# Optimization experiments

Measured on AMD Instinct MI355X. Metric: run time of the kernel, lower is better.

## Reference

```python
import jax, jax.numpy as jnp
import numpy as np

# static config (matches init_kwargs)
C = 64            # dim_split = dim // 4
DIM = 256
HID = 128         # int(dim//4 * mlp_ratio), mlp_ratio=2
S = 64            # state_dim
NH, HD = 16, 4    # GA: num_heads = C // head_dim, head_dim = 4
AK, AP = 11, 5    # att_kernel, att_padding
B, H, W = 8, 28, 28


def conv2d(x, w, pad, stride=1, groups=1, bias=None):
    out = jax.lax.conv_general_dilated(
        x, w, (stride, stride), pad, feature_group_count=groups,
        dimension_numbers=('NCHW', 'OIHW', 'NCHW'))
    if bias is not None:
        out = out + bias[None, :, None, None]
    return out


def pw(x, w, b=None):  # 1x1 conv, w: (O, Cin)
    y = jnp.einsum('oc,bchw->bohw', w, x)
    return y if b is None else y + b[None, :, None, None]


def bn(x, p, eps=1e-5):  # eval-mode BatchNorm2d; p: (4, C) = gamma, beta, mean, var
    g, b, m, v = p
    s = g / jnp.sqrt(v + eps)
    return (x - m[None, :, None, None]) * s[None, :, None, None] + b[None, :, None, None]


def relu6(x):
    return jnp.minimum(jax.nn.relu(x), 6.0)


def maxpool3(x):  # 3x3, stride 1, pad 1
    return jax.lax.reduce_window(x, -jnp.inf, jax.lax.max, (1, 1, 3, 3), (1, 1, 1, 1),
                                 [(0, 0), (0, 0), (1, 1), (1, 1)])


def blurpool(x):  # antialiased_cnns.BlurPool(channels, stride=3), filt_size=4
    a = np.array([1.0, 3.0, 3.0, 1.0])
    filt = np.outer(a, a)
    filt = filt / filt.sum()
    c = x.shape[1]
    w = jnp.asarray(np.tile(filt[None, None], (c, 1, 1, 1)), x.dtype)
    xp = jnp.pad(x, ((0, 0), (0, 0), (1, 2), (1, 2)), mode='reflect')
    return conv2d(xp, w, [(0, 0), (0, 0)], stride=3, groups=c)


def h_transform(x):
    b, c, hs, ws = x.shape
    x = jnp.pad(x, ((0, 0), (0, 0), (0, 0), (0, ws))).reshape(b, c, -1)[..., :-ws]
    return x.reshape(b, c, hs, 2 * ws - 1)


def inv_h_transform(x):
    b, c, hs, _ = x.shape
    x = jnp.pad(x.reshape(b, c, -1), ((0, 0), (0, 0), (0, hs)))
    return x.reshape(b, c, hs, 2 * hs)[..., :hs]


def v_transform(x):
    return h_transform(x.transpose(0, 1, 3, 2)).transpose(0, 1, 3, 2)


def inv_v_transform(x):
    return inv_h_transform(x.transpose(0, 1, 3, 2)).transpose(0, 1, 3, 2)


def _forward(x, dw1_w, dw1_b, bn_dw1, f1_w, f1_b, f2_w, f2_b, g_w, g_b, bn_g,
             dw2_w, dw2_b, hatt1_w, vatt1_w, hatt2_w, vatt2_w, bn_mra,
             bcdt_w, ssd_dw_w, hz_w, out_w, A_param, D_param,
             qkv_w, proj_w, bn_norm4, mlp1_w, bn_mlp, mlp2_w, bn_norm1):
    shortcut = x
    x1, x2, x3, x4 = jnp.split(x, 4, axis=1)

    # --- branch 1: dwconv + star-gated MLP ---
    x1o = bn(conv2d(x1, dw1_w, [(3, 3), (3, 3)], groups=C, bias=dw1_b), bn_dw1)
    x1 = relu6(pw(x1o, f1_w, f1_b)) * pw(x1o, f2_w, f2_b)
    x1 = conv2d(bn(pw(x1, g_w, g_b), bn_g), dw2_w, [(3, 3), (3, 3)], groups=C, bias=dw2_b)

    # --- branch 2: MRA ---
    xt = blurpool(maxpool3(x2))  # (B, C, 10, 10)
    xh1 = conv2d(xt, hatt1_w, [(AP, AP), (1, 1)], groups=C)
    xw1 = conv2d(xt, vatt1_w, [(1, 1), (AP, AP)], groups=C)
    xh2 = inv_h_transform(conv2d(h_transform(xt), hatt2_w, [(AP, AP), (1, 1)], groups=C))
    xw2 = inv_v_transform(conv2d(v_transform(xt), vatt2_w, [(1, 1), (AP, AP)], groups=C))
    att = jax.nn.sigmoid(bn(xh1 + xw1 + xh2 + xw2, bn_mra))
    hs, ws = att.shape[-2], att.shape[-1]
    ri = (jnp.arange(H) * hs) // H  # nearest-neighbor upsampling indices
    ci = (jnp.arange(W) * ws) // W
    x2 = x2 * att[:, :, ri][:, :, :, ci]

    # --- branch 3: HSMSSD (hidden-state-mixer SSD) ---
    L = H * W
    xs = x3.reshape(B, C, L)
    bcdt = conv2d(jnp.einsum('oc,bcl->bol', bcdt_w, xs).reshape(B, 3 * S, H, W),
                  ssd_dw_w, [(1, 1), (1, 1)], groups=3 * S).reshape(B, 3 * S, L)
    Bm, Cm, dt = jnp.split(bcdt, 3, axis=1)              # each (B, S, L)
    A = jax.nn.softmax(dt + A_param[None, :, None], axis=-1)
    h = jnp.einsum('bcl,bsl->bcs', xs, A * Bm)           # (B, C, S)
    h_, z = jnp.split(jnp.einsum('oc,bcs->bos', hz_w, h), 2, axis=1)
    h_ = jnp.einsum('oc,bcs->bos', out_w, h_ * jax.nn.silu(z) + h_ * D_param)
    x3 = jnp.einsum('bcs,bsl->bcl', h_, Cm).reshape(B, C, H, W)

    # --- branch 4: GA full attention + BN residual (stage == 3) ---
    t = x4.reshape(B, C, L).transpose(0, 2, 1)           # (B, N, C)
    qkv = (t @ qkv_w.T).reshape(B, L, 3, NH, HD).transpose(2, 0, 3, 1, 4)
    q, k, v = qkv[0], qkv[1], qkv[2]
    attn = jax.nn.softmax(jnp.einsum('bhnd,bhmd->bhnm', q, k) * HD ** -0.5, axis=-1)
    o = jnp.einsum('bhnm,bhmd->bhnd', attn, v).transpose(0, 2, 1, 3).reshape(B, L, NH * HD)
    x4 = bn(x4 + (o @ proj_w.T).transpose(0, 2, 1).reshape(B, C, H, W), bn_norm4)

    # --- merge + MLP ---
    xa = jnp.concatenate([x1, x2, x3, x4], axis=1)
    m = pw(jax.nn.relu(bn(pw(xa, mlp1_w), bn_mlp)), mlp2_w)
    return shortcut + bn(m, bn_norm1)


def setup_inputs() -> dict:
    key = jax.random.key(0)
    ks = iter(jax.random.split(key, 64))

    def w(shape, s=0.05):
        return jax.random.normal(next(ks), shape, dtype=jnp.float32) * s

    def bnp(c):
        g = 1.0 + 0.1 * jax.random.normal(next(ks), (c,), dtype=jnp.float32)
        b = 0.1 * jax.random.normal(next(ks), (c,), dtype=jnp.float32)
        m = 0.1 * jax.random.normal(next(ks), (c,), dtype=jnp.float32)
        v = 0.5 + jax.random.uniform(next(ks), (c,), dtype=jnp.float32)
        return jnp.stack([g, b, m, v])

    return dict(
        x=jax.random.normal(next(ks), (B, DIM, H, W), dtype=jnp.float32),
        dw1_w=w((C, 1, 7, 7), 0.1), dw1_b=w((C,), 0.02), bn_dw1=bnp(C),
        f1_w=w((HID, C)), f1_b=w((HID,), 0.02),
        f2_w=w((HID, C)), f2_b=w((HID,), 0.02),
        g_w=w((C, HID)), g_b=w((C,), 0.02), bn_g=bnp(C),
        dw2_w=w((C, 1, 7, 7), 0.1), dw2_b=w((C,), 0.02),
        hatt1_w=w((C, 1, AK, 3), 0.1), vatt1_w=w((C, 1, 3, AK), 0.1),
        hatt2_w=w((C, 1, AK, 3), 0.1), vatt2_w=w((C, 1, 3, AK), 0.1),
        bn_mra=bnp(C),
        bcdt_w=w((3 * S, C)), ssd_dw_w=w((3 * S, 1, 3, 3), 0.1),
        hz_w=w((2 * C, C)), out_w=w((C, C)),
        A_param=jax.random.uniform(next(ks), (S,), dtype=jnp.float32, minval=1.0, maxval=16.0),
        D_param=jnp.ones((1,), dtype=jnp.float32),
        qkv_w=w((3 * NH * HD, C)), proj_w=w((C, NH * HD)),
        bn_norm4=bnp(C),
        mlp1_w=w((HID, DIM)), bn_mlp=bnp(HID), mlp2_w=w((DIM, HID)),
        bn_norm1=bnp(DIM),
    )


def reference(x, dw1_w, dw1_b, bn_dw1, f1_w, f1_b, f2_w, f2_b, g_w, g_b, bn_g,
              dw2_w, dw2_b, hatt1_w, vatt1_w, hatt2_w, vatt2_w, bn_mra,
              bcdt_w, ssd_dw_w, hz_w, out_w, A_param, D_param,
              qkv_w, proj_w, bn_norm4, mlp1_w, bn_mlp, mlp2_w, bn_norm1):
    return _forward(x, dw1_w, dw1_b, bn_dw1, f1_w, f1_b, f2_w, f2_b, g_w, g_b, bn_g,
                    dw2_w, dw2_b, hatt1_w, vatt1_w, hatt2_w, vatt2_w, bn_mra,
                    bcdt_w, ssd_dw_w, hz_w, out_w, A_param, D_param,
                    qkv_w, proj_w, bn_norm4, mlp1_w, bn_mlp, mlp2_w, bn_norm1)
```

## Files before the change

kernel.cpp:

```cpp
#include <hip/hip_runtime.h>
#include <hip/hip_bf16.h>
#include <math.h>

#define DEV __device__ __forceinline__

constexpr int B=8, C=64, DIM=256, HID=128, S=64, NH=16, HD=4, LPIX=784;
constexpr int NPIX = B*LPIX;
constexpr int CH   = (NPIX+255)/256;
constexpr int QB   = 12*((NPIX+511)/512);

constexpr size_t OFF_X1O = 0;
constexpr size_t OFF_T1  = OFF_X1O + (size_t)B*C*LPIX;
constexpr size_t OFF_T2  = OFF_T1  + (size_t)B*HID*LPIX;
constexpr size_t OFF_XA  = OFF_T2  + (size_t)B*C*LPIX;
constexpr size_t OFF_BC2 = OFF_XA  + (size_t)B*DIM*LPIX;
constexpr size_t OFF_WGT = OFF_BC2 + (size_t)B*192*LPIX;
constexpr size_t OFF_H   = OFF_WGT + (size_t)B*S*LPIX;
constexpr size_t OFF_HO  = OFF_H   + (size_t)4*B*C*S;
constexpr size_t OFF_QKV = OFF_HO  + (size_t)B*C*S;
constexpr size_t OFF_O   = OFF_QKV + (size_t)3*B*NH*LPIX*HD;
constexpr size_t OFF_LS  = OFF_O   + (size_t)4*B*LPIX*C;
constexpr size_t OFF_MID = OFF_LS  + (size_t)4*B*NH*LPIX;

DEV float bnorm(float x, const float* p, int c, int nc){
  float g=p[c], bb=p[nc+c], m=p[2*nc+c], v=p[3*nc+c];
  return (x-m)*(g*rsqrtf(v+1e-5f))+bb;
}
DEV int refl(int p){ int k=p-1; if(k<0)k=-k; if(k>27)k=54-k; return k; }

DEV bool upix(int blk, int tid, int ngroups, int& grp, int& b, int& l){
  grp = blk % ngroups;
  int gidx = (blk/ngroups)*256 + tid;
  if(gidx >= NPIX) return false;
  b = gidx / LPIX; l = gidx % LPIX;
  return true;
}

DEV void body_dw1t(int bc, int tid, float* xs, const float* X, const float* w, const float* bias, const float* bnp, float* out){
  int c = bc & 63, b = bc >> 6;
  const float* xp = X + ((size_t)(b*DIM+c))*LPIX;
  for(int i=tid;i<34*34;i+=256) xs[i]=0.f;
  __syncthreads();
  for(int i=tid;i<LPIX;i+=256){ int y=i/28, x=i%28; xs[(y+3)*34+(x+3)]=xp[i]; }
  __syncthreads();
  const float* wc = w + (size_t)c*49;
  float bs = bias[c];
  for(int i=tid;i<LPIX;i+=256){
    int y=i/28, x=i%28;
    float s = bs;
    #pragma unroll
    for(int ky=0;ky<7;ky++){
      #pragma unroll
      for(int kx=0;kx<7;kx++)
        s += xs[(y+ky)*34 + x+kx]*wc[ky*7+kx];
    }
    out[((size_t)(b*C+c))*LPIX + i] = bnorm(s,bnp,c,C);
  }
}

DEV void body_branch2(int bc, int tid, float* smem, const float* X,
                      const float* h1w,const float* v1w,const float* h2w,const float* v2w,
                      const float* bnp, float* xa){
  int c = bc & 63, b = bc >> 6;
  float* xs  = smem;
  float* mp  = smem+LPIX;
  float* xt  = smem+2*LPIX;
  float* attv= smem+2*LPIX+100;
  const float* xp = X + ((size_t)(b*DIM+64+c))*LPIX;
  for(int i=tid;i<LPIX;i+=256) xs[i]=xp[i];
  __syncthreads();
  for(int i=tid;i<LPIX;i+=256){
    int y=i/28, x=i%28;
    float m=-1e30f;
    for(int dy=-1;dy<=1;dy++){ int iy=y+dy; if(iy<0||iy>=28) continue;
      for(int dx=-1;dx<=1;dx++){ int ix=x+dx; if(ix<0||ix>=28) continue;
        m=fmaxf(m,xs[iy*28+ix]); } }
    mp[i]=m;
  }
  __syncthreads();
  if(tid<100){
    int ii=tid/10, j=tid%10;
    const float fw[4]={0.125f,0.375f,0.375f,0.125f};
    float s=0;
    for(int ky=0;ky<4;ky++){ int rr=refl(3*ii+ky);
      for(int kx=0;kx<4;kx++){ int cc=refl(3*j+kx);
        s += fw[ky]*fw[kx]*mp[rr*28+cc]; } }
    xt[tid]=s;
  }
  __syncthreads();
  if(tid<100){
    int r=tid/10, j=tid%10;
    float s=0;
    for(int kh=0;kh<11;kh++){ int a=r+kh-5; if(a<0||a>=10) continue;
      for(int kw=0;kw<3;kw++){ int b2=j+kw-1; if(b2<0||b2>=10) continue;
        s+=xt[a*10+b2]*h1w[(size_t)c*33+kh*3+kw]; } }
    for(int kh=0;kh<3;kh++){ int a=r+kh-1; if(a<0||a>=10) continue;
      for(int kw=0;kw<11;kw++){ int b2=j+kw-5; if(b2<0||b2>=10) continue;
        s+=xt[a*10+b2]*v1w[(size_t)c*33+kh*11+kw]; } }
    { int t=20*r+j; int r2=t/19, j2=t%19;
      for(int kh=0;kh<11;kh++){ int a=r2+kh-5; if(a<0||a>=10) continue;
        for(int kw=0;kw<3;kw++){ int b2=j2+kw-1; if(b2<0||b2>=19) continue;
          int i2=19*a+b2; int row=i2/20, col=i2%20;
          if(col<10) s+=xt[row*10+col]*h2w[(size_t)c*33+kh*3+kw]; } } }
    { int t=20*j+r; int p=t%19, q=t/19;
      for(int kh=0;kh<3;kh++){ int a=p+kh-1; if(a<0||a>=19) continue;
        for(int kw=0;kw<11;kw++){ int b2=q+kw-5; if(b2<0||b2>=10) continue;
          int i2=19*b2+a; int row=i2/20, col=i2%20;
          if(col<10) s+=xt[col*10+row]*v2w[(size_t)c*33+kh*11+kw]; } } }
    s = bnorm(s,bnp,c,C);
    attv[tid] = 1.f/(1.f+__expf(-s));
  }
  __syncthreads();
  float* dst = xa + ((size_t)(b*DIM+64+c))*LPIX;
  for(int i=tid;i<LPIX;i+=256){
    int y=i/28, x=i%28;
    float a = attv[((y*10)/28)*10 + (x*10)/28];
    dst[i] = xs[i]*a;
  }
}

DEV void body_qkv(int blk, int tid, const float* X, const float* w, float* qkvb){
  int og = blk % 12;
  int p0 = (blk/12)*512 + tid;
  if(p0 >= NPIX) return;
  int o0 = og*16;
  int b0 = p0/LPIX, l0 = p0%LPIX;
  int p1 = p0 + 256;
  bool has1 = p1 < NPIX;
  int b1 = has1 ? p1/LPIX : b0, l1 = has1 ? p1%LPIX : l0;
  const float* xp0 = X + ((size_t)(b0*DIM+192))*LPIX + l0;
  const float* xp1 = X + ((size_t)(b1*DIM+192))*LPIX + l1;
  float s0[16], s1[16];
  #pragma unroll
  for(int t=0;t<16;t++){ s0[t]=0.f; s1[t]=0.f; }
  for(int c=0;c<C;c+=4){
    float a0=xp0[(size_t)c*LPIX],     a1=xp0[(size_t)(c+1)*LPIX],
          a2=xp0[(size_t)(c+2)*LPIX], a3=xp0[(size_t)(c+3)*LPIX];
    float e0=xp1[(size_t)c*LPIX],     e1=xp1[(size_t)(c+1)*LPIX],
          e2=xp1[(size_t)(c+2)*LPIX], e3=xp1[(size_t)(c+3)*LPIX];
    #pragma unroll
    for(int t=0;t<16;t++){
      const float* wr = w + (size_t)(o0+t)*C + c;
      float w0=wr[0], w1=wr[1], w2=wr[2], w3=wr[3];
      s0[t] += w0*a0 + w1*a1 + w2*a2 + w3*a3;
      s1[t] += w0*e0 + w1*e1 + w2*e2 + w3*e3;
    }
  }
  int which=o0>>6, head0=(o0&63)>>2;
  #pragma unroll
  for(int t4=0;t4<4;t4++){
    float4* dst = (float4*)(qkvb + (size_t)which*B*NH*LPIX*HD + ((size_t)((b0*NH+head0+t4)*LPIX+l0))*HD);
    *dst = make_float4(s0[4*t4],s0[4*t4+1],s0[4*t4+2],s0[4*t4+3]);
  }
  if(has1){
    #pragma unroll
    for(int t4=0;t4<4;t4++){
      float4* dst = (float4*)(qkvb + (size_t)which*B*NH*LPIX*HD + ((size_t)((b1*NH+head0+t4)*LPIX+l1))*HD);
      *dst = make_float4(s1[4*t4],s1[4*t4+1],s1[4*t4+2],s1[4*t4+3]);
    }
  }
}

DEV void body_bcdtssd(int blk, int tid, float* smem, const float* X, const float* w, const float* dww,
                      float* bc2, float* wgt){
  int b = blk/48, og = blk%48; int o0=og*4;
  float* bc1s = smem;
  float* dts  = smem + 4*LPIX;
  const float* xp = X + ((size_t)(b*DIM+128))*LPIX;
  {
    int l0=tid, l1=tid+256, l2=tid+512;
    float acc0[4]={0,0,0,0}, acc1[4]={0,0,0,0}, acc2[4]={0,0,0,0};
    for(int c=0;c<C;c+=4){
      float x00=xp[(size_t)c*LPIX+l0],     x01=xp[(size_t)(c+1)*LPIX+l0],
            x02=xp[(size_t)(c+2)*LPIX+l0], x03=xp[(size_t)(c+3)*LPIX+l0];
      float x10=xp[(size_t)c*LPIX+l1],     x11=xp[(size_t)(c+1)*LPIX+l1],
            x12=xp[(size_t)(c+2)*LPIX+l1], x13=xp[(size_t)(c+3)*LPIX+l1];
      float x20=xp[(size_t)c*LPIX+l2],     x21=xp[(size_t)(c+1)*LPIX+l2],
            x22=xp[(size_t)(c+2)*LPIX+l2], x23=xp[(size_t)(c+3)*LPIX+l2];
      #pragma unroll
      for(int t=0;t<4;t++){
        const float* wr = w + (size_t)(o0+t)*C + c;
        float w0=wr[0], w1=wr[1], w2=wr[2], w3=wr[3];
        acc0[t] += w0*x00 + w1*x01 + w2*x02 + w3*x03;
        acc1[t] += w0*x10 + w1*x11 + w2*x12 + w3*x13;
        acc2[t] += w0*x20 + w1*x21 + w2*x22 + w3*x23;
      }
    }
    #pragma unroll
    for(int t=0;t<4;t++){
      bc1s[t*LPIX+l0]=acc0[t];
      bc1s[t*LPIX+l1]=acc1[t];
      bc1s[t*LPIX+l2]=acc2[t];
    }
    if(tid<16){
      int l=768+tid;
      float a0=0,a1=0,a2=0,a3=0;
      for(int c=0;c<C;c+=4){
        float x0=xp[(size_t)c*LPIX+l],     x1=xp[(size_t)(c+1)*LPIX+l],
              x2=xp[(size_t)(c+2)*LPIX+l], x3=xp[(size_t)(c+3)*LPIX+l];
        const float* w0p = w + (size_t)(o0+0)*C + c;
        const float* w1p = w + (size_t)(o0+1)*C + c;
        const float* w2p = w + (size_t)(o0+2)*C + c;
        const float* w3p = w + (size_t)(o0+3)*C + c;
        a0 += w0p[0]*x0 + w0p[1]*x1 + w0p[2]*x2 + w0p[3]*x3;
        a1 += w1p[0]*x0 + w1p[1]*x1 + w1p[2]*x2 + w1p[3]*x3;
        a2 += w2p[0]*x0 + w2p[1]*x1 + w2p[2]*x2 + w2p[3]*x3;
        a3 += w3p[0]*x0 + w3p[1]*x1 + w3p[2]*x2 + w3p[3]*x3;
      }
      bc1s[0*LPIX+l]=a0; bc1s[1*LPIX+l]=a1; bc1s[2*LPIX+l]=a2; bc1s[3*LPIX+l]=a3;
    }
  }
  __syncthreads();
  for(int i=tid;i<4*LPIX;i+=256){
    int oo=i/LPIX, l=i%LPIX; int y=l/28, x=l%28;
    const float* p = bc1s + oo*LPIX;
    const float* wk = dww + (size_t)(o0+oo)*9;
    float s=0;
    for(int ky=0;ky<3;ky++){ int iy=y+ky-1; if(iy<0||iy>=28) continue;
      for(int kx=0;kx<3;kx++){ int ix=x+kx-1; if(ix<0||ix>=28) continue;
        s += p[iy*28+ix]*wk[ky*3+kx]; } }
    dts[i] = s;
    bc2[((size_t)(b*192+o0+oo))*LPIX + l] = s;
  }
  if(og >= 32){
    __syncthreads();
    int wv = tid>>6, lane = tid&63;
    float* row = dts + wv*LPIX;
    float mx = -1e30f;
    for(int l=lane;l<LPIX;l+=64) mx = fmaxf(mx, row[l]);
    for(int off=32;off;off>>=1) mx = fmaxf(mx, __shfl_xor(mx,off));
    float sum=0;
    for(int l=lane;l<LPIX;l+=64){ float e=__expf(row[l]-mx); row[l]=e; sum+=e; }
    for(int off=32;off;off>>=1) sum += __shfl_xor(sum,off);
    float inv = 1.f/sum;
    int s_ = o0-128+wv;
    float* wp = wgt + ((size_t)(b*S+s_))*LPIX;
    for(int l=lane;l<LPIX;l+=64) wp[l] = row[l]*inv;
  }
}

DEV void body_attn(int blk, int tid, float4* ks, float4* vs, const float* qkvb,
                   float* ob, float* lsb){
  int bh = blk >> 2, ms = blk & 3;
  int b = bh>>4, h = bh&15;
  const float4* q4 = (const float4*)(qkvb + (size_t)bh*LPIX*HD);
  const float4* k4 = (const float4*)(qkvb + (size_t)(B*NH + bh)*LPIX*HD) + ms*196;
  const float4* v4 = (const float4*)(qkvb + (size_t)(2*B*NH + bh)*LPIX*HD) + ms*196;
  for(int i=tid;i<196;i+=256){ ks[i]=k4[i]; vs[i]=v4[i]; }
  __syncthreads();
  const float SC = 0.5f*1.44269504f;
  float* obp = ob + (size_t)ms*B*LPIX*C;
  float* lsq = lsb + (size_t)ms*B*NH*LPIX + (size_t)bh*LPIX;

  float4 q[3];
  #pragma unroll
  for(int j=0;j<3;j++){
    float4 t = q4[tid + 256*j];
    q[j] = make_float4(t.x*SC, t.y*SC, t.z*SC, t.w*SC);
  }
  float l0[3]={0,0,0}, l1[3]={0,0,0};
  float ax0[3]={0,0,0}, ax1[3]={0,0,0};
  float ay0[3]={0,0,0}, ay1[3]={0,0,0};
  float az0[3]={0,0,0}, az1[3]={0,0,0};
  float aw0[3]={0,0,0}, aw1[3]={0,0,0};
  for(int m=0;m<196;m+=2){
    float4 k0=ks[m], k1=ks[m+1];
    float4 v0=vs[m], v1=vs[m+1];
    #pragma unroll
    for(int j=0;j<3;j++){
      float s0 = q[j].x*k0.x + q[j].y*k0.y + q[j].z*k0.z + q[j].w*k0.w;
      float s1 = q[j].x*k1.x + q[j].y*k1.y + q[j].z*k1.z + q[j].w*k1.w;
      float p0 = __builtin_amdgcn_exp2f(s0);
      float p1 = __builtin_amdgcn_exp2f(s1);
      l0[j]+=p0;        l1[j]+=p1;
      ax0[j]+=p0*v0.x;  ax1[j]+=p1*v1.x;
      ay0[j]+=p0*v0.y;  ay1[j]+=p1*v1.y;
      az0[j]+=p0*v0.z;  az1[j]+=p1*v1.z;
      aw0[j]+=p0*v0.w;  aw1[j]+=p1*v1.w;
    }
  }
  #pragma unroll
  for(int j=0;j<3;j++){
    int r = tid + 256*j;
    *(float4*)(obp + ((size_t)(b*LPIX+r))*C + h*4) =
        make_float4(ax0[j]+ax1[j], ay0[j]+ay1[j], az0[j]+az1[j], aw0[j]+aw1[j]);
    lsq[r] = l0[j]+l1[j];
  }
  if(tid < 16){
    int r = 768 + tid;
    float4 t = q4[r];
    float4 qq = make_float4(t.x*SC,t.y*SC,t.z*SC,t.w*SC);
    float ls=0; float4 a=make_float4(0,0,0,0);
    for(int m=0;m<196;m++){
      float4 kv=ks[m], vv=vs[m];
      float sc = qq.x*kv.x+qq.y*kv.y+qq.z*kv.z+qq.w*kv.w;
      float p = __builtin_amdgcn_exp2f(sc);
      ls+=p; a.x+=p*vv.x; a.y+=p*vv.y; a.z+=p*vv.z; a.w+=p*vv.w;
    }
    *(float4*)(obp + ((size_t)(b*LPIX+r))*C + h*4) = a;
    lsq[r] = ls;
  }
}

DEV void body_star(int blk, int tid, const float* x1o, const float* f1w,const float* f1b,const float* f2w,const float* f2b,float* t1){
  int jg, b, l; if(!upix(blk, tid, 32, jg, b, l)) return;
  int j0=jg*4;
  const float* xp = x1o + (size_t)b*C*LPIX + l;
  float a[4], g[4];
  for(int t=0;t<4;t++){ a[t]=f1b[j0+t]; g[t]=f2b[j0+t]; }
  for(int c=0;c<C;c++){
    float xv = xp[(size_t)c*LPIX];
    for(int t=0;t<4;t++){ a[t]+=f1w[(size_t)(j0+t)*C+c]*xv; g[t]+=f2w[(size_t)(j0+t)*C+c]*xv; }
  }
  for(int t=0;t<4;t++){
    float av = fminf(fmaxf(a[t],0.f),6.f);
    t1[((size_t)(b*HID+j0+t))*LPIX + l] = av*g[t];
  }
}

DEV void body_gproj(int blk, int tid, const float* t1, const float* gw,const float* gb,const float* bnp,float* t2){
  int cg, b, l; if(!upix(blk, tid, 4, cg, b, l)) return;
  int c0=cg*16;
  const float* tp = t1 + (size_t)b*HID*LPIX + l;
  float s[16];
  #pragma unroll
  for(int t=0;t<16;t++) s[t]=gb[c0+t];
  for(int j=0;j<HID;j++){
    float xv = tp[(size_t)j*LPIX];
    #pragma unroll
    for(int t=0;t<16;t++) s[t]+=gw[(size_t)(c0+t)*HID+j]*xv;
  }
  #pragma unroll
  for(int t=0;t<16;t++) t2[((size_t)(b*C+c0+t))*LPIX + l]=bnorm(s[t],bnp,c0+t,C);
}

DEV void body_x4(int blk, int tid, const float* X, const float* ob, const float* lsb,
                 const float* projw, const float* bnp, float* xa){
  int cg, b, l; if(!upix(blk, tid, 4, cg, b, l)) return;
  int c0=cg*16;
  const float* p0 = ob + ((size_t)(b*LPIX+l))*C;
  const float* p1 = p0 + (size_t)B*LPIX*C;
  const float* p2 = p1 + (size_t)B*LPIX*C;
  const float* p3 = p2 + (size_t)B*LPIX*C;
  float s[16];
  #pragma unroll
  for(int t=0;t<16;t++) s[t]=0.f;
  for(int h=0;h<NH;h++){
    size_t li = ((size_t)(b*NH+h))*LPIX + l;
    float lsum = lsb[li] + lsb[(size_t)B*NH*LPIX+li] + lsb[(size_t)2*B*NH*LPIX+li] + lsb[(size_t)3*B*NH*LPIX+li];
    float iv = 1.f/lsum;
    float4 q0=*(const float4*)(p0+h*4), q1=*(const float4*)(p1+h*4),
           q2=*(const float4*)(p2+h*4), q3=*(const float4*)(p3+h*4);
    float ov0=(q0.x+q1.x+q2.x+q3.x)*iv;
    float ov1=(q0.y+q1.y+q2.y+q3.y)*iv;
    float ov2=(q0.z+q1.z+q2.z+q3.z)*iv;
    float ov3=(q0.w+q1.w+q2.w+q3.w)*iv;
    const float* pw = projw + h*4;
    #pragma unroll
    for(int t=0;t<16;t++){
      const float* pr = pw + (size_t)(c0+t)*C;
      s[t] += pr[0]*ov0 + pr[1]*ov1 + pr[2]*ov2 + pr[3]*ov3;
    }
  }
  #pragma unroll
  for(int t=0;t<16;t++){
    float v = s[t] + X[((size_t)(b*DIM+192+c0+t))*LPIX + l];
    xa[((size_t)(b*DIM+192+c0+t))*LPIX + l] = bnorm(v,bnp,c0+t,C);
  }
}

DEV void body_h(int blk, int tid, float* smem, const float* X, const float* wgt, const float* bc2, float* hq){
  int b = blk >> 6, sub = blk & 63;
  int tile = sub >> 2, qq = sub & 3;
  int ct = (tile>>2)*16, st = (tile&3)*16;
  int l0 = qq*196;
  float (*Xs)[197] = (float(*)[197])smem;
  float (*Ws)[197] = (float(*)[197])(smem + 16*197);
  for(int i=tid;i<16*196;i+=256){
    int r=i/196, col=i%196;
    Xs[r][col] = X[((size_t)(b*DIM+128+ct+r))*LPIX + l0 + col];
    Ws[r][col] = wgt[((size_t)(b*S+st+r))*LPIX + l0 + col]
               * bc2[((size_t)(b*192+st+r))*LPIX + l0 + col];
  }
  __syncthreads();
  int tc = tid>>4, ts = tid&15;
  float acc=0;
  #pragma unroll 4
  for(int l=0;l<196;l++) acc += Xs[tc][l]*Ws[ts][l];
  hq[(size_t)qq*B*C*S + ((size_t)(b*C+ct+tc))*S + st+ts] = acc;
}

DEV void body_dw2t(int bc, int tid, float* xs, const float* t2, const float* w, const float* bias, float* xa){
  int c = bc & 63, b = bc >> 6;
  const float* tp = t2 + ((size_t)(b*C+c))*LPIX;
  for(int i=tid;i<34*34;i+=256) xs[i]=0.f;
  __syncthreads();
  for(int i=tid;i<LPIX;i+=256){ int y=i/28, x=i%28; xs[(y+3)*34+(x+3)]=tp[i]; }
  __syncthreads();
  const float* wc = w + (size_t)c*49;
  float bs = bias[c];
  for(int i=tid;i<LPIX;i+=256){
    int y=i/28, x=i%28;
    float s = bs;
    #pragma unroll
    for(int ky=0;ky<7;ky++){
      #pragma unroll
      for(int kx=0;kx<7;kx++)
        s += xs[(y+ky)*34 + x+kx]*wc[ky*7+kx];
    }
    xa[((size_t)(b*DIM+c))*LPIX + i] = s;
  }
}

DEV void body_mixho(int blk, int tid, float* smem, const float* hq, const float* hzw,
                    const float* Dp, const float* outw, float* ho){
  int b = blk >> 3, st = (blk & 7) * 8;
  float (*hs2)[8] = (float(*)[8])smem;
  float (*g1s)[8] = (float(*)[8])(smem + C*8);
  for(int i=tid;i<C*8;i+=256){
    int k=i>>3, si=i&7;
    size_t off = ((size_t)(b*C+k))*S + st + si;
    hs2[k][si] = hq[off] + hq[(size_t)B*C*S+off] + hq[(size_t)2*B*C*S+off] + hq[(size_t)3*B*C*S+off];
  }
  __syncthreads();
  float D = Dp[0];
  for(int i=tid;i<C*8;i+=256){
    int c=i>>3, si=i&7;
    float hv=0, zv=0;
    for(int k=0;k<C;k++){ float x=hs2[k][si]; hv+=hzw[(size_t)c*C+k]*x; zv+=hzw[(size_t)(C+c)*C+k]*x; }
    float sil = zv/(1.f+__expf(-zv));
    g1s[c][si]=hv*sil+hv*D;
  }
  __syncthreads();
  for(int i=tid;i<C*8;i+=256){
    int c=i>>3, si=i&7;
    float acc=0;
    for(int k=0;k<C;k++) acc+=outw[(size_t)c*C+k]*g1s[k][si];
    ho[((size_t)(b*C+c))*S + st + si]=acc;
  }
}

DEV void body_x3(int blk, int tid, const float* ho, const float* bc2, float* xa){
  int cg, b, l; if(!upix(blk, tid, 16, cg, b, l)) return;
  int c0=cg*4;
  const float* hp = ho + (size_t)(b*C+c0)*S;
  const float* cm = bc2 + ((size_t)(b*192+64))*LPIX + l;
  float s[4]={0,0,0,0};
  for(int s_=0;s_<S;s_++){
    float cv = cm[(size_t)s_*LPIX];
    for(int t=0;t<4;t++) s[t] += hp[(size_t)t*S+s_]*cv;
  }
  for(int t=0;t<4;t++)
    xa[((size_t)(b*DIM+128+c0+t))*LPIX + l] = s[t];
}

__global__ void k_s1(const float* X,
                     const float* bcdt_w, const float* ssd_dw, float* bc2, float* wgt,
                     const float* h1w,const float* v1w,const float* h2w,const float* v2w,const float* bn_mra,
                     const float* qkv_w, float* qkvb,
                     const float* dw1_w,const float* dw1_b,const float* bn_dw1,
                     float* xa, float* x1o){
  __shared__ float smem[8*LPIX];
  int blk = blockIdx.x, tid = threadIdx.x;
  if(blk < 384)            body_bcdtssd(blk, tid, smem, X, bcdt_w, ssd_dw, bc2, wgt);
  else if(blk < 896)       body_branch2(blk-384, tid, smem, X, h1w,v1w,h2w,v2w, bn_mra, xa);
  else if(blk < 896+QB)    body_qkv(blk-896, tid, X, qkv_w, qkvb);
  else                     body_dw1t(blk-(896+QB), tid, smem, X, dw1_w, dw1_b, bn_dw1, x1o);
}

__global__ void k_s2(const float* qkvb, float* ob, float* lsb,
                     const float* x1o, const float* f1w,const float* f1b,const float* f2w,const float* f2b, float* t1,
                     const float* X, const float* wgt, const float* bc2, float* hq){
  __shared__ float4 smem4[1576];
  float* smem = (float*)smem4;
  int blk = blockIdx.x, tid = threadIdx.x;
  if(blk < 512)            body_attn(blk, tid, smem4, smem4+196, qkvb, ob, lsb);
  else if(blk < 512+32*CH) body_star(blk-512, tid, x1o, f1w,f1b,f2w,f2b, t1);
  else                     body_h(blk-(512+32*CH), tid, smem, X, wgt, bc2, hq);
}

__global__ void k_s3(const float* t1, const float* gw,const float* gb,const float* bn_g, float* t2,
                     const float* X, const float* ob, const float* lsb,
                     const float* projw, const float* bn_n4, float* xa,
                     const float* hq, const float* hzw, const float* Dp, const float* outw, float* ho){
  __shared__ float smem[2*C*8];
  int blk = blockIdx.x, tid = threadIdx.x;
  if(blk < 64)           body_mixho(blk, tid, smem, hq, hzw, Dp, outw, ho);
  else if(blk < 64+4*CH) body_gproj(blk-64, tid, t1, gw, gb, bn_g, t2);
  else                   body_x4(blk-(64+4*CH), tid, X, ob, lsb, projw, bn_n4, xa);
}

__global__ void k_s4(const float* t2, const float* dw2_w, const float* dw2_b, float* xa,
                     const float* ho, const float* bc2){
  __shared__ float smem[34*34];
  int blk = blockIdx.x, tid = threadIdx.x;
  if(blk < 512) body_dw2t(blk, tid, smem, t2, dw2_w, dw2_b, xa);
  else          body_x3(blk-512, tid, ho, bc2, xa);
}

__global__ void k_mid(const float* xa, const float* m1w, const float* bnp, float* mid){
  int jg, b, l; if(!upix(blockIdx.x, threadIdx.x, 32, jg, b, l)) return;
  int j0=jg*4;
  const float* xp = xa + (size_t)b*DIM*LPIX + l;
  float s[4]={0,0,0,0};
  for(int c=0;c<DIM;c++){
    float xv=xp[(size_t)c*LPIX];
    for(int t=0;t<4;t++) s[t]+=m1w[(size_t)(j0+t)*DIM+c]*xv;
  }
  for(int t=0;t<4;t++)
    mid[((size_t)(b*HID+j0+t))*LPIX + l] = fmaxf(bnorm(s[t],bnp,j0+t,HID),0.f);
}

__global__ void k_out(const float* X, const float* mid, const float* m2w, const float* bnp, float* out){
  int cg, b, l; if(!upix(blockIdx.x, threadIdx.x, 32, cg, b, l)) return;
  int c0=cg*8;
  const float* mp_ = mid + (size_t)b*HID*LPIX + l;
  float s[8]={0,0,0,0,0,0,0,0};
  for(int j=0;j<HID;j++){
    float mv=mp_[(size_t)j*LPIX];
    for(int t=0;t<8;t++) s[t]+=m2w[(size_t)(c0+t)*HID+j]*mv;
  }
  for(int t=0;t<8;t++){
    size_t oi = ((size_t)(b*DIM+c0+t))*LPIX + l;
    out[oi] = bnorm(s[t],bnp,c0+t,DIM) + X[oi];
  }
}

extern "C" void kernel_launch(void* const* d_in, const int* in_sizes, int n_in,
                              void* d_out, int out_size, void* d_ws, size_t ws_size,
                              hipStream_t stream) {
  const float* X      = (const float*)d_in[0];
  const float* dw1_w  = (const float*)d_in[1];
  const float* dw1_b  = (const float*)d_in[2];
  const float* bn_dw1 = (const float*)d_in[3];
  const float* f1_w   = (const float*)d_in[4];
  const float* f1_b   = (const float*)d_in[5];
  const float* f2_w   = (const float*)d_in[6];
  const float* f2_b   = (const float*)d_in[7];
  const float* g_w    = (const float*)d_in[8];
  const float* g_b    = (const float*)d_in[9];
  const float* bn_g   = (const float*)d_in[10];
  const float* dw2_w  = (const float*)d_in[11];
  const float* dw2_b  = (const float*)d_in[12];
  const float* hatt1w = (const float*)d_in[13];
  const float* vatt1w = (const float*)d_in[14];
  const float* hatt2w = (const float*)d_in[15];
  const float* vatt2w = (const float*)d_in[16];
  const float* bn_mra = (const float*)d_in[17];
  const float* bcdt_w = (const float*)d_in[18];
  const float* ssd_dw = (const float*)d_in[19];
  const float* hz_w   = (const float*)d_in[20];
  const float* out_w  = (const float*)d_in[21];
  const float* D_p    = (const float*)d_in[23];
  const float* qkv_w  = (const float*)d_in[24];
  const float* proj_w = (const float*)d_in[25];
  const float* bn_n4  = (const float*)d_in[26];
  const float* mlp1_w = (const float*)d_in[27];
  const float* bn_mlp = (const float*)d_in[28];
  const float* mlp2_w = (const float*)d_in[29];
  const float* bn_n1  = (const float*)d_in[30];

  float* ws   = (float*)d_ws;
  float* x1o  = ws+OFF_X1O;  float* t1  = ws+OFF_T1;  float* t2  = ws+OFF_T2;
  float* xa   = ws+OFF_XA;   float* bc2 = ws+OFF_BC2; float* wgt = ws+OFF_WGT;
  float* hq   = ws+OFF_H;    float* ho  = ws+OFF_HO;  float* qkvb= ws+OFF_QKV;
  float* ob   = ws+OFF_O;    float* lsb = ws+OFF_LS;  float* mid = ws+OFF_MID;

  dim3 blk(256);

  k_s1 <<<dim3(896+QB+512),blk,0,stream>>>(X, bcdt_w, ssd_dw, bc2, wgt,
                                     hatt1w,vatt1w,hatt2w,vatt2w,bn_mra,
                                     qkv_w, qkvb, dw1_w,dw1_b,bn_dw1, xa, x1o);
  k_s2 <<<dim3(512+32*CH+512),blk,0,stream>>>(qkvb, ob, lsb,
                                     x1o, f1_w,f1_b,f2_w,f2_b, t1,
                                     X, wgt, bc2, hq);
  k_s3 <<<dim3(64+8*CH),blk,0,stream>>>(t1, g_w,g_b,bn_g, t2,
                                     X, ob, lsb, proj_w, bn_n4, xa,
                                     hq, hz_w, D_p, out_w, ho);
  k_s4 <<<dim3(512+16*CH),blk,0,stream>>>(t2, dw2_w, dw2_b, xa, ho, bc2);
  k_mid<<<dim3(32*CH),blk,0,stream>>>(xa,mlp1_w,bn_mlp,mid);
  k_out<<<dim3(32*CH),blk,0,stream>>>(X,mid,mlp2_w,bn_n1,(float*)d_out);
}
```

Measured before the change: 283.4 us.

## Shrink shared memory and add launch bounds to raise k_s1/k_s2 occupancy

In the bcdt/ssd body, the softmax rows are now computed one at a time with block-wide max and sum reductions. This lets that stage use about 5 rows of shared memory instead of 8. The body_h GEMM tile is split into two 98-column halves so k_s2 needs half the shared buffer. Both kernels get __launch_bounds__(256,8) so more blocks fit per CU. The trade-offs are extra __syncthreads in the softmax and tile loops, and a risk of register spills under the tighter register cap.

```diff
diff --git a/kernel.cpp b/kernel.cpp
--- a/kernel.cpp
+++ b/kernel.cpp
@@ -165,7 +165,8 @@
                       float* bc2, float* wgt){
   int b = blk/48, og = blk%48; int o0=og*4;
   float* bc1s = smem;
-  float* dts  = smem + 4*LPIX;
+  float* dts1 = smem + 4*LPIX;
+  float* red  = smem + 5*LPIX;
   const float* xp = X + ((size_t)(b*DIM+128))*LPIX;
   {
     int l0=tid, l1=tid+256, l2=tid+512;
@@ -211,31 +212,50 @@
     }
   }
   __syncthreads();
-  for(int i=tid;i<4*LPIX;i+=256){
-    int oo=i/LPIX, l=i%LPIX; int y=l/28, x=l%28;
-    const float* p = bc1s + oo*LPIX;
-    const float* wk = dww + (size_t)(o0+oo)*9;
-    float s=0;
-    for(int ky=0;ky<3;ky++){ int iy=y+ky-1; if(iy<0||iy>=28) continue;
-      for(int kx=0;kx<3;kx++){ int ix=x+kx-1; if(ix<0||ix>=28) continue;
-        s += p[iy*28+ix]*wk[ky*3+kx]; } }
-    dts[i] = s;
-    bc2[((size_t)(b*192+o0+oo))*LPIX + l] = s;
-  }
-  if(og >= 32){
-    __syncthreads();
+  if(og < 32){
+    for(int i=tid;i<4*LPIX;i+=256){
+      int oo=i/LPIX, l=i%LPIX; int y=l/28, x=l%28;
+      const float* p = bc1s + oo*LPIX;
+      const float* wk = dww + (size_t)(o0+oo)*9;
+      float s=0;
+      for(int ky=0;ky<3;ky++){ int iy=y+ky-1; if(iy<0||iy>=28) continue;
+        for(int kx=0;kx<3;kx++){ int ix=x+kx-1; if(ix<0||ix>=28) continue;
+          s += p[iy*28+ix]*wk[ky*3+kx]; } }
+      bc2[((size_t)(b*192+o0+oo))*LPIX + l] = s;
+    }
+  } else {
     int wv = tid>>6, lane = tid&63;
-    float* row = dts + wv*LPIX;
-    float mx = -1e30f;
-    for(int l=lane;l<LPIX;l+=64) mx = fmaxf(mx, row[l]);
-    for(int off=32;off;off>>=1) mx = fmaxf(mx, __shfl_xor(mx,off));
-    float sum=0;
-    for(int l=lane;l<LPIX;l+=64){ float e=__expf(row[l]-mx); row[l]=e; sum+=e; }
-    for(int off=32;off;off>>=1) sum += __shfl_xor(sum,off);
-    float inv = 1.f/sum;
-    int s_ = o0-128+wv;
-    float* wp = wgt + ((size_t)(b*S+s_))*LPIX;
-    for(int l=lane;l<LPIX;l+=64) wp[l] = row[l]*inv;
+    for(int oo=0;oo<4;oo++){
+      const float* p = bc1s + oo*LPIX;
+      const float* wk = dww + (size_t)(o0+oo)*9;
+      float lmax=-1e30f;
+      for(int i=tid;i<LPIX;i+=256){
+        int y=i/28, x=i%28;
+        float s=0;
+        for(int ky=0;ky<3;ky++){ int iy=y+ky-1; if(iy<0||iy>=28) continue;
+          for(int kx=0;kx<3;kx++){ int ix=x+kx-1; if(ix<0||ix>=28) continue;
+            s += p[iy*28+ix]*wk[ky*3+kx]; } }
+        dts1[i]=s;
+        lmax=fmaxf(lmax,s);
+      }
+      for(int off=32;off;off>>=1) lmax=fmaxf(lmax,__shfl_xor(lmax,off));
+      if(lane==0) red[wv]=lmax;
+      __syncthreads();
+      float bmax = fmaxf(fmaxf(red[0],red[1]),fmaxf(red[2],red[3]));
+      float lsum=0;
+      for(int i=tid;i<LPIX;i+=256){
+        float e=__expf(dts1[i]-bmax);
+        dts1[i]=e; lsum+=e;
+      }
+      for(int off=32;off;off>>=1) lsum += __shfl_xor(lsum,off);
+      if(lane==0) red[4+wv]=lsum;
+      __syncthreads();
+      float inv = 1.f/(red[4]+red[5]+red[6]+red[7]);
+      int s_ = o0-128+oo;
+      float* wp = wgt + ((size_t)(b*S+s_))*LPIX;
+      for(int i=tid;i<LPIX;i+=256) wp[i] = dts1[i]*inv;
+      __syncthreads();
+    }
   }
 }
 
@@ -373,20 +393,24 @@
   int b = blk >> 6, sub = blk & 63;
   int tile = sub >> 2, qq = sub & 3;
   int ct = (tile>>2)*16, st = (tile&3)*16;
-  int l0 = qq*196;
-  float (*Xs)[197] = (float(*)[197])smem;
-  float (*Ws)[197] = (float(*)[197])(smem + 16*197);
-  for(int i=tid;i<16*196;i+=256){
-    int r=i/196, col=i%196;
-    Xs[r][col] = X[((size_t)(b*DIM+128+ct+r))*LPIX + l0 + col];
-    Ws[r][col] = wgt[((size_t)(b*S+st+r))*LPIX + l0 + col]
-               * bc2[((size_t)(b*192+st+r))*LPIX + l0 + col];
-  }
-  __syncthreads();
+  float (*Xs)[99] = (float(*)[99])smem;
+  float (*Ws)[99] = (float(*)[99])(smem + 16*99);
   int tc = tid>>4, ts = tid&15;
   float acc=0;
-  #pragma unroll 4
-  for(int l=0;l<196;l++) acc += Xs[tc][l]*Ws[ts][l];
+  #pragma unroll
+  for(int half=0;half<2;half++){
+    int lb = qq*196 + half*98;
+    for(int i=tid;i<16*98;i+=256){
+      int r=i/98, col=i%98;
+      Xs[r][col] = X[((size_t)(b*DIM+128+ct+r))*LPIX + lb + col];
+      Ws[r][col] = wgt[((size_t)(b*S+st+r))*LPIX + lb + col]
+                 * bc2[((size_t)(b*192+st+r))*LPIX + lb + col];
+    }
+    __syncthreads();
+    #pragma unroll 7
+    for(int l=0;l<98;l++) acc += Xs[tc][l]*Ws[ts][l];
+    __syncthreads();
+  }
   hq[(size_t)qq*B*C*S + ((size_t)(b*C+ct+tc))*S + st+ts] = acc;
 }
 
@@ -454,13 +478,13 @@
     xa[((size_t)(b*DIM+128+c0+t))*LPIX + l] = s[t];
 }
 
-__global__ void k_s1(const float* X,
+__global__ void __launch_bounds__(256,8) k_s1(const float* X,
                      const float* bcdt_w, const float* ssd_dw, float* bc2, float* wgt,
                      const float* h1w,const float* v1w,const float* h2w,const float* v2w,const float* bn_mra,
                      const float* qkv_w, float* qkvb,
                      const float* dw1_w,const float* dw1_b,const float* bn_dw1,
                      float* xa, float* x1o){
-  __shared__ float smem[8*LPIX];
+  __shared__ float smem[5*LPIX+8];
   int blk = blockIdx.x, tid = threadIdx.x;
   if(blk < 384)            body_bcdtssd(blk, tid, smem, X, bcdt_w, ssd_dw, bc2, wgt);
   else if(blk < 896)       body_branch2(blk-384, tid, smem, X, h1w,v1w,h2w,v2w, bn_mra, xa);
@@ -468,10 +492,10 @@
   else                     body_dw1t(blk-(896+QB), tid, smem, X, dw1_w, dw1_b, bn_dw1, x1o);
 }
 
-__global__ void k_s2(const float* qkvb, float* ob, float* lsb,
+__global__ void __launch_bounds__(256,8) k_s2(const float* qkvb, float* ob, float* lsb,
                      const float* x1o, const float* f1w,const float* f1b,const float* f2w,const float* f2b, float* t1,
                      const float* X, const float* wgt, const float* bc2, float* hq){
-  __shared__ float4 smem4[1576];
+  __shared__ float4 smem4[792];
   float* smem = (float*)smem4;
   int blk = blockIdx.x, tid = threadIdx.x;
   if(blk < 512)            body_attn(blk, tid, smem4, smem4+196, qkvb, ob, lsb);
```

Result: slower. 326.1 us (+15.1%).
